# Kernel optimization log

Hardware: AMD Instinct MI355X
Metric: run time of the kernel (lower is better)

## Reference

```python
import jax, jax.numpy as jnp
import numpy as np

H = 128      # hidden_channels
G = 512      # number of graphs in the batch
NEG_SLOPE = 0.2


def _seg_sum(x, idx, n):
    return jax.ops.segment_sum(x, idx, num_segments=n)


def _sage(x_src, x_dst, ei, Wl, bl, Wr):
    # PyG SAGEConv: lin_l(mean_j x_j) + lin_r(x_i); lin_l has bias, lin_r does not.
    s, d = ei[0], ei[1]
    n = x_dst.shape[0]
    agg = _seg_sum(x_src[s], d, n)
    cnt = _seg_sum(jnp.ones((ei.shape[1],), x_src.dtype), d, n)
    mean = agg / jnp.maximum(cnt, 1.0)[:, None]
    return mean @ Wl + bl + x_dst @ Wr


def _gat(x_src, x_dst, ei, Ws, Wd, a_s, a_d, b):
    # PyG GATConv (heads=1, add_self_loops=False, bipartite): segment softmax over dst.
    s, d = ei[0], ei[1]
    n = x_dst.shape[0]
    hs = x_src @ Ws                                  # [N_src, H]
    hd = x_dst @ Wd                                  # [N_dst, H]
    logit = jax.nn.leaky_relu((hs @ a_s)[s] + (hd @ a_d)[d], NEG_SLOPE)
    m = jax.ops.segment_max(logit, d, num_segments=n)
    e = jnp.exp(logit - m[d])
    z = _seg_sum(e, d, n)
    alpha = e / jnp.maximum(z[d], 1e-16)
    return _seg_sum(alpha[:, None] * hs[s], d, n) + b


def _gcn(x, ei, W, b):
    # PyG GCNConv with add_self_loops=True, normalize=True (same src/dst node type).
    s, d = ei[0], ei[1]
    n = x.shape[0]
    deg = _seg_sum(jnp.ones((ei.shape[1],), x.dtype), d, n) + 1.0  # +1 self loop
    dis = jax.lax.rsqrt(deg)
    h = x @ W
    norm = dis[s] * dis[d]
    out = _seg_sum(norm[:, None] * h[s], d, n) + (dis * dis)[:, None] * h
    return out + b


def _pool(x, b):
    s = _seg_sum(x, b, G)
    c = _seg_sum(jnp.ones((x.shape[0],), x.dtype), b, G)
    return s / jnp.maximum(c, 1.0)[:, None]


def setup_inputs() -> dict:
    key = jax.random.key(0)
    ks = iter(jax.random.split(key, 80))
    scale = 1.0 / np.sqrt(H)

    def nrm(shape, sc=scale):
        return jax.random.normal(next(ks), shape, jnp.float32) * sc

    def edges(e, n_src, n_dst):
        src = jax.random.randint(next(ks), (e,), 0, n_src, jnp.int32)
        dst = jax.random.randint(next(ks), (e,), 0, n_dst, jnp.int32)
        return jnp.stack([src, dst])

    def batch(n):
        return jnp.sort(jax.random.randint(next(ks), (n,), 0, G, jnp.int32))

    N_CD, N_SEQ, N_ANNO, N_RANGE, N_MD = 100000, 80000, 80000, 80000, 50000
    inp = {
        'x_cd': nrm((N_CD, H), 1.0), 'x_seq': nrm((N_SEQ, H), 1.0),
        'x_anno': nrm((N_ANNO, H), 1.0), 'x_range': nrm((N_RANGE, H), 1.0),
        'x_md': nrm((N_MD, H), 1.0),
        'ei_seq': edges(160000, N_CD, N_SEQ),
        'ei_anno': edges(200000, N_CD, N_ANNO),
        'ei_range': edges(200000, N_CD, N_RANGE),
        'ei_comp': edges(300000, N_MD, N_CD),
        'ei_cc': edges(300000, N_CD, N_CD),
        'ei_mm': edges(150000, N_MD, N_MD),
        'b_cd': batch(N_CD), 'b_seq': batch(N_SEQ), 'b_anno': batch(N_ANNO),
        'b_range': batch(N_RANGE), 'b_md': batch(N_MD),
    }
    # per-layer stacked params (leading axis = 2 layers)
    for nm, shp in [('Wsl_seq', (2, H, H)), ('bs_seq', (2, H)), ('Wsr_seq', (2, H, H)),
                    ('Wsl_anno', (2, H, H)), ('bs_anno', (2, H)), ('Wsr_anno', (2, H, H)),
                    ('Wg_comp_s', (2, H, H)), ('Wg_comp_d', (2, H, H)),
                    ('ag_comp_s', (2, H)), ('ag_comp_d', (2, H)), ('bg_comp', (2, H)),
                    ('Wg_range_s', (2, H, H)), ('Wg_range_d', (2, H, H)),
                    ('ag_range_s', (2, H)), ('ag_range_d', (2, H)), ('bg_range', (2, H)),
                    ('Wc_cc', (2, H, H)), ('bc_cc', (2, H)),
                    ('Wc_mm', (2, H, H)), ('bc_mm', (2, H)),
                    ('lin1_W', (5 * H, H)), ('lin1_b', (H,)),
                    ('lin2_W', (H, 1)), ('lin2_b', (1,))]:
        inp[nm] = nrm(shp)
    return inp


def reference(x_cd, x_seq, x_anno, x_range, x_md,
              ei_seq, ei_anno, ei_range, ei_comp, ei_cc, ei_mm,
              b_cd, b_seq, b_anno, b_range, b_md,
              Wsl_seq, bs_seq, Wsr_seq, Wsl_anno, bs_anno, Wsr_anno,
              Wg_comp_s, Wg_comp_d, ag_comp_s, ag_comp_d, bg_comp,
              Wg_range_s, Wg_range_d, ag_range_s, ag_range_d, bg_range,
              Wc_cc, bc_cc, Wc_mm, bc_mm,
              lin1_W, lin1_b, lin2_W, lin2_b):
    for l in range(2):
        # HeteroConv aggr='sum': CD receives GAT(MD->CD) + GCN(CD->CD)
        n_cd = (_gat(x_md, x_cd, ei_comp, Wg_comp_s[l], Wg_comp_d[l],
                     ag_comp_s[l], ag_comp_d[l], bg_comp[l])
                + _gcn(x_cd, ei_cc, Wc_cc[l], bc_cc[l]))
        n_seq = _sage(x_cd, x_seq, ei_seq, Wsl_seq[l], bs_seq[l], Wsr_seq[l])
        n_anno = _sage(x_cd, x_anno, ei_anno, Wsl_anno[l], bs_anno[l], Wsr_anno[l])
        n_range = _gat(x_cd, x_range, ei_range, Wg_range_s[l], Wg_range_d[l],
                       ag_range_s[l], ag_range_d[l], bg_range[l])
        n_md = _gcn(x_md, ei_mm, Wc_mm[l], bc_mm[l])
        x_cd, x_seq, x_anno, x_range, x_md = (
            jax.nn.relu(n_cd), jax.nn.relu(n_seq), jax.nn.relu(n_anno),
            jax.nn.relu(n_range), jax.nn.relu(n_md))
    emb = jnp.concatenate([_pool(x_cd, b_cd), _pool(x_seq, b_seq),
                           _pool(x_anno, b_anno), _pool(x_range, b_range),
                           _pool(x_md, b_md)], axis=-1)        # [G, 5H]
    h = jax.nn.relu(emb @ lin1_W + lin1_b)  # Dropout(0.7) is identity in eval
    return (h @ lin2_W + lin2_b).reshape(-1)  # [G]
```

## Files before the change

kernel.cpp:

```cpp
#include <hip/hip_runtime.h>

#define HD 128
#define GNUM 512
#define RPB 520
#define IDXCAP 1024

typedef __attribute__((ext_vector_type(8))) short short8v;
typedef __attribute__((ext_vector_type(4))) float f32x4;

__device__ __forceinline__ void split1(float a, short& h, short& l) {
  unsigned u = __float_as_uint(a);
  unsigned hb = (u + 0x7FFFu + ((u >> 16) & 1u)) & 0xFFFF0000u;
  h = (short)(hb >> 16);
  float rest = a - __uint_as_float(hb);
  unsigned u2 = __float_as_uint(rest);
  l = (short)((u2 + 0x7FFFu + ((u2 >> 16) & 1u)) >> 16);
}

struct WTab { const float* p[8]; };
__global__ __launch_bounds__(256) void k_split_w(WTab tab, short* __restrict__ whi,
                                                 short* __restrict__ wlo)
{
  int m = blockIdx.x >> 6;
  int i = (blockIdx.x & 63) * 256 + threadIdx.x;
  const float* W = tab.p[m >> 1] + (m & 1) * 16384;
  int k = i >> 7, n = i & 127;
  short h, l;
  split1(W[k * 128 + n], h, l);
  whi[m * 16384 + n * 128 + k] = h;
  wlo[m * 16384 + n * 128 + k] = l;
}

#define CF_LD 132
__device__ __forceinline__ void gemm_body(
    int blockid, char* smem, int* idxbuf,
    const float* __restrict__ A1, const short* __restrict__ WH1, const short* __restrict__ WL1,
    const int* __restrict__ grp, const int* __restrict__ gcol,
    const float* __restrict__ A2, const short* __restrict__ WH2, const short* __restrict__ WL2,
    float* __restrict__ C, const float* __restrict__ bias, int N, int relu,
    const float* __restrict__ avec, float* __restrict__ adot)
{
  short* Ah = (short*)smem;
  short* Al = Ah + 64 * 136;
  float* Cf = (float*)smem;

  const int t = threadIdx.x;
  const int row0 = blockid * 64;
  const int lane = t & 63, wid = t >> 6;
  const int g = lane >> 4, cn = lane & 15;
  const int colbase = wid * 32;

  f32x4 zero = {0.f, 0.f, 0.f, 0.f};
  f32x4 acc[4][2];
#pragma unroll
  for (int rt = 0; rt < 4; ++rt) { acc[rt][0] = zero; acc[rt][1] = zero; }

  float4 a2reg[8];
  if (A2) {
    const float4* A4 = (const float4*)(A2 + (size_t)row0 * 128);
#pragma unroll
    for (int i = 0; i < 8; ++i) {
      int f4 = t + i * 256;
      int row = f4 >> 5;
      a2reg[i] = (row0 + row < N) ? A4[f4] : make_float4(0.f, 0.f, 0.f, 0.f);
    }
  }

  auto stageA = [&](const float* __restrict__ A) {
    const float4* A4 = (const float4*)(A + (size_t)row0 * 128);
#pragma unroll
    for (int i = 0; i < 8; ++i) {
      int f4 = t + i * 256;
      int row = f4 >> 5, c4 = f4 & 31;
      float4 v = make_float4(0.f, 0.f, 0.f, 0.f);
      if (row0 + row < N) v = A4[f4];
      short4 h, l;
      split1(v.x, h.x, l.x); split1(v.y, h.y, l.y);
      split1(v.z, h.z, l.z); split1(v.w, h.w, l.w);
      *(short4*)(Ah + row * 136 + c4 * 4) = h;
      *(short4*)(Al + row * 136 + c4 * 4) = l;
    }
  };

  auto stageA_gather = [&](const float* __restrict__ X, int e_lo) {
#pragma unroll
    for (int i = 0; i < 8; ++i) {
      int f4 = t + i * 256;
      int row = f4 >> 5, ln = f4 & 31;
      int r = row0 + row;
      float4 s = make_float4(0.f, 0.f, 0.f, 0.f);
      int e0 = 0, e1 = 0;
      if (r < N) { e0 = grp[r]; e1 = grp[r + 1]; }
      for (int e = e0; e < e1; ++e) {
        int off = e - e_lo;
        int c = (off < IDXCAP) ? idxbuf[off] : gcol[e];
        float4 v = *(const float4*)(X + (size_t)c * 128 + ln * 4);
        s.x += v.x; s.y += v.y; s.z += v.z; s.w += v.w;
      }
      float inv = 1.f / fmaxf((float)(e1 - e0), 1.f);
      short4 h, l;
      split1(s.x * inv, h.x, l.x); split1(s.y * inv, h.y, l.y);
      split1(s.z * inv, h.z, l.z); split1(s.w * inv, h.w, l.w);
      *(short4*)(Ah + row * 136 + ln * 4) = h;
      *(short4*)(Al + row * 136 + ln * 4) = l;
    }
  };

  auto accum = [&](const short* __restrict__ WH, const short* __restrict__ WL) {
    short8v bhi[2][4], blo[2][4];
#pragma unroll
    for (int ct = 0; ct < 2; ++ct)
#pragma unroll
      for (int kg = 0; kg < 4; ++kg) {
        size_t o = (size_t)(colbase + ct * 16 + cn) * 128 + kg * 32 + g * 8;
        bhi[ct][kg] = *(const short8v*)(WH + o);
        blo[ct][kg] = *(const short8v*)(WL + o);
      }
#pragma unroll
    for (int kg = 0; kg < 4; ++kg) {
#pragma unroll
      for (int rt = 0; rt < 4; ++rt) {
        const int ao = (rt * 16 + cn) * 136 + kg * 32 + g * 8;
        const short8v ah = *(const short8v*)(Ah + ao);
        const short8v al = *(const short8v*)(Al + ao);
#pragma unroll
        for (int ct = 0; ct < 2; ++ct) {
          acc[rt][ct] = __builtin_amdgcn_mfma_f32_16x16x32_bf16(ah, bhi[ct][kg], acc[rt][ct], 0, 0, 0);
          acc[rt][ct] = __builtin_amdgcn_mfma_f32_16x16x32_bf16(al, bhi[ct][kg], acc[rt][ct], 0, 0, 0);
          acc[rt][ct] = __builtin_amdgcn_mfma_f32_16x16x32_bf16(ah, blo[ct][kg], acc[rt][ct], 0, 0, 0);
        }
      }
    }
  };

  if (grp) {
    const int row_end = min(row0 + 64, N);
    const int e_lo = grp[row0];
    const int cnt = min(grp[row_end] - e_lo, IDXCAP);
    for (int k = t; k < cnt; k += 256) idxbuf[k] = gcol[e_lo + k];
    __syncthreads();
    stageA_gather(A1, e_lo);
  } else {
    stageA(A1);
  }
  __syncthreads();
  accum(WH1, WL1);
  if (A2) {
    __syncthreads();
#pragma unroll
    for (int i = 0; i < 8; ++i) {
      int f4 = t + i * 256;
      int row = f4 >> 5, c4 = f4 & 31;
      short4 h, l;
      split1(a2reg[i].x, h.x, l.x); split1(a2reg[i].y, h.y, l.y);
      split1(a2reg[i].z, h.z, l.z); split1(a2reg[i].w, h.w, l.w);
      *(short4*)(Ah + row * 136 + c4 * 4) = h;
      *(short4*)(Al + row * 136 + c4 * 4) = l;
    }
    __syncthreads();
    accum(WH2, WL2);
  }
  __syncthreads();

  if (avec) {
    float* part = (float*)smem;
    const float av0 = avec[colbase + cn];
    const float av1 = avec[colbase + 16 + cn];
#pragma unroll
    for (int rt = 0; rt < 4; ++rt)
#pragma unroll
      for (int r = 0; r < 4; ++r) {
        float p = fmaf(acc[rt][1][r], av1, acc[rt][0][r] * av0);
#pragma unroll
        for (int o = 1; o < 16; o <<= 1) p += __shfl_xor(p, o);
        if (cn == 0) part[wid * 64 + rt * 16 + g * 4 + r] = p;
      }
    __syncthreads();
    if (t < 64) {
      int row = row0 + t;
      if (row < N) adot[row] = part[t] + part[64 + t] + part[128 + t] + part[192 + t];
    }
    __syncthreads();
  }

#pragma unroll
  for (int rt = 0; rt < 4; ++rt)
#pragma unroll
    for (int ct = 0; ct < 2; ++ct)
#pragma unroll
      for (int r = 0; r < 4; ++r)
        Cf[(rt * 16 + g * 4 + r) * CF_LD + colbase + ct * 16 + cn] = acc[rt][ct][r];
  __syncthreads();

  float4* C4 = (float4*)(C + (size_t)row0 * 128);
#pragma unroll
  for (int i = 0; i < 8; ++i) {
    int f4 = t + i * 256;
    int row = f4 >> 5, c4 = f4 & 31;
    if (row0 + row < N) {
      float4 v = *(const float4*)(Cf + row * CF_LD + c4 * 4);
      if (bias) {
        float4 bv = *(const float4*)(bias + c4 * 4);
        v.x += bv.x; v.y += bv.y; v.z += bv.z; v.w += bv.w;
      }
      if (relu) {
        v.x = fmaxf(v.x, 0.f); v.y = fmaxf(v.y, 0.f);
        v.z = fmaxf(v.z, 0.f); v.w = fmaxf(v.w, 0.f);
      }
      C4[f4] = v;
    }
  }
}

__global__ __launch_bounds__(256) void k_gemm_mfma(
    const float* A1, const short* WH1, const short* WL1,
    const int* grp, const int* gcol,
    const float* A2, const short* WH2, const short* WL2,
    float* C, const float* bias, int N, int relu,
    const float* avec, float* adot)
{
  __shared__ char smem[64 * 136 * 2 * 2];
  __shared__ int idxbuf[IDXCAP];
  gemm_body(blockIdx.x, smem, idxbuf, A1, WH1, WL1, grp, gcol,
            A2, WH2, WL2, C, bias, N, relu, avec, adot);
}

struct SPair {
  const float* A1[2]; const short* WH1[2]; const short* WL1[2];
  const int* grp[2]; const int* gcol[2];
  const float* A2[2]; const short* WH2[2]; const short* WL2[2];
  float* C[2]; const float* bias[2]; int N[2]; int bo;
};
__global__ __launch_bounds__(256) void k_gemm_sage2(SPair p)
{
  __shared__ char smem[64 * 136 * 2 * 2];
  __shared__ int idxbuf[IDXCAP];
  int ty = (blockIdx.x >= p.bo) ? 1 : 0;
  int bid = blockIdx.x - (ty ? p.bo : 0);
  gemm_body(bid, smem, idxbuf, p.A1[ty], p.WH1[ty], p.WL1[ty], p.grp[ty], p.gcol[ty],
            p.A2[ty], p.WH2[ty], p.WL2[ty], p.C[ty], p.bias[ty], p.N[ty], 1,
            nullptr, nullptr);
}

__global__ void k_rowdot(const float* __restrict__ x, const float* __restrict__ a,
                         float* __restrict__ out, int N)
{
  int wid = blockIdx.x * 4 + (threadIdx.x >> 6);
  int lane = threadIdx.x & 63;
  if (wid >= N) return;
  float2 xv = ((const float2*)x)[(size_t)wid * 64 + lane];
  float2 av = ((const float2*)a)[lane];
  float v = fmaf(xv.y, av.y, xv.x * av.x);
#pragma unroll
  for (int o = 32; o > 0; o >>= 1) v += __shfl_down(v, o);
  if (lane == 0) out[wid] = v;
}

struct MTab { const float* W[4]; const float* a[4]; };
__global__ __launch_bounds__(128) void k_matvec4(MTab tb, float* __restrict__ wv)
{
  __shared__ float as[128];
  int m = blockIdx.x, i = threadIdx.x;
  as[i] = tb.a[m][i];
  __syncthreads();
  const float* W = tb.W[m];
  float v = 0.f;
  for (int j = 0; j < 128; ++j) v = fmaf(W[i * 128 + j], as[j], v);
  wv[m * 128 + i] = v;
}

struct HTab { const int* key[6]; int* cnt[6]; unsigned short* rank[6]; int bo[7]; int n[6]; };
__global__ void k_hist_rank_all(HTab tb) {
  int bi = blockIdx.x, ty = 0;
  while (ty < 5 && bi >= tb.bo[ty + 1]) ++ty;
  int i = (bi - tb.bo[ty]) * 256 + threadIdx.x;
  if (i < tb.n[ty])
    tb.rank[ty][i] = (unsigned short)atomicAdd(&tb.cnt[ty][tb.key[ty][i]], 1);
}

struct FTab { const int* es[6]; const int* ed[6]; const int* rp[6];
              const unsigned short* rank[6]; int* col[6]; int bo[7]; int n[6]; };
__global__ void k_fill_all(FTab tb) {
  int bi = blockIdx.x, ty = 0;
  while (ty < 5 && bi >= tb.bo[ty + 1]) ++ty;
  int e = (bi - tb.bo[ty]) * 256 + threadIdx.x;
  if (e >= tb.n[ty]) return;
  int p = tb.rp[ty][tb.ed[ty][e]] + (int)tb.rank[ty][e];
  tb.col[ty][p] = tb.es[ty][e];
}

struct STab { int* rp[6]; int* bs[6]; int n[6]; int bo[7]; };

__global__ __launch_bounds__(256) void k_scan_partial_all(STab tb) {
  __shared__ int red[256];
  int bi = blockIdx.x, ty = 0;
  while (ty < 5 && bi >= tb.bo[ty + 1]) ++ty;
  int lb = bi - tb.bo[ty];
  const int* rp = tb.rp[ty];
  const int N = tb.n[ty];
  const int t = threadIdx.x, base = lb * 4096;
  int s = 0;
  for (int i = t; i < 4096; i += 256) {
    int idx = base + i;
    if (idx < N) s += rp[idx];
  }
  red[t] = s;
  __syncthreads();
  for (int ofs = 128; ofs > 0; ofs >>= 1) {
    if (t < ofs) red[t] += red[t + ofs];
    __syncthreads();
  }
  if (t == 0) tb.bs[ty][lb] = red[0];
}

__global__ __launch_bounds__(256) void k_scan_bsums_all(STab tb) {
  __shared__ int sh[256];
  const int ty = blockIdx.x;
  const int nb = (tb.n[ty] + 4095) / 4096;
  const int t = threadIdx.x;
  int v = (t < nb) ? tb.bs[ty][t] : 0;
  sh[t] = v;
  __syncthreads();
  for (int ofs = 1; ofs < 256; ofs <<= 1) {
    int u = (t >= ofs) ? sh[t - ofs] : 0;
    __syncthreads();
    sh[t] += u;
    __syncthreads();
  }
  if (t < nb) tb.bs[ty][t] = sh[t] - v;
  if (t == 255) tb.rp[ty][tb.n[ty]] = sh[255];
}

__global__ __launch_bounds__(256) void k_scan_final_all(STab tb) {
  __shared__ int sh[4096 + 256];
  __shared__ int tsum[256];
  int bi = blockIdx.x, ty = 0;
  while (ty < 5 && bi >= tb.bo[ty + 1]) ++ty;
  int lb = bi - tb.bo[ty];
  int* rp = tb.rp[ty];
  const int N = tb.n[ty];
  const int t = threadIdx.x, base = lb * 4096;
  auto mp = [](int i) { return i + (i >> 4); };
#pragma unroll
  for (int i = 0; i < 16; ++i) {
    int idx = base + i * 256 + t;
    sh[mp(i * 256 + t)] = (idx < N) ? rp[idx] : 0;
  }
  __syncthreads();
  int s = 0;
#pragma unroll
  for (int j = 0; j < 16; ++j) s += sh[mp(t * 16 + j)];
  tsum[t] = s;
  __syncthreads();
  for (int ofs = 1; ofs < 256; ofs <<= 1) {
    int u = (t >= ofs) ? tsum[t - ofs] : 0;
    __syncthreads();
    tsum[t] += u;
    __syncthreads();
  }
  int pre = tsum[t] - s + tb.bs[ty][lb];
#pragma unroll
  for (int j = 0; j < 16; ++j) {
    int v = sh[mp(t * 16 + j)];
    sh[mp(t * 16 + j)] = pre;
    pre += v;
  }
  __syncthreads();
#pragma unroll
  for (int i = 0; i < 16; ++i) {
    int idx = base + i * 256 + t;
    if (idx < N) rp[idx] = sh[mp(i * 256 + t)];
  }
}

struct BTab { const int* b[5]; int n[5]; };
__global__ __launch_bounds__(512) void k_runptr(BTab tb, int* __restrict__ rpb_all) {
  const int ty = blockIdx.x;
  const int* b = tb.b[ty];
  const int N = tb.n[ty];
  const int t = threadIdx.x;
  int lo = 0, hi = N;
  while (lo < hi) {
    int mid = (lo + hi) >> 1;
    if (b[mid] < t) lo = mid + 1; else hi = mid;
  }
  rpb_all[ty * RPB + t] = lo;
  if (t == 0) rpb_all[ty * RPB + GNUM] = N;
}

struct DTab { const int* rp[2]; float* dis[2]; int n[2]; int bo[3]; };
__global__ void k_dis2(DTab tb) {
  int bi = blockIdx.x, ty = (bi >= tb.bo[1]) ? 1 : 0;
  int n = (bi - tb.bo[ty]) * 256 + threadIdx.x;
  if (n < tb.n[ty]) tb.dis[ty][n] = rsqrtf((float)(tb.rp[ty][n + 1] - tb.rp[ty][n]) + 1.f);
}

__global__ void k_gcn_gather(const int* __restrict__ rp, const int* __restrict__ col,
                             const float* __restrict__ dis, const float* __restrict__ h,
                             const float* addin, const float* __restrict__ b,
                             float* out, int N,
                             const float* __restrict__ dvec, float* __restrict__ dout)
{
  int node = blockIdx.x * 4 + (threadIdx.x >> 6);
  if (node >= N) return;
  int lane = threadIdx.x & 63;
  int s0 = rp[node], deg = rp[node + 1] - s0;
  float rd = dis[node];
  const float2* h2 = (const float2*)h;
  float2 hself = h2[(size_t)node * 64 + lane];
  float2 bv = ((const float2*)b)[lane];
  float ad0 = 0.f, ad1 = 0.f;
  if (addin) {
    float2 a2 = ((const float2*)addin)[(size_t)node * 64 + lane];
    ad0 = a2.x; ad1 = a2.y;
  }
  float a0 = 0.f, a1 = 0.f, b0 = 0.f, b1 = 0.f;
  for (int base = 0; base < deg; base += 64) {
    int m = min(64, deg - base);
    int c = 0; float dv = 0.f;
    if (lane < m) { c = col[s0 + base + lane]; dv = dis[c]; }
    int j = 0;
    for (; j + 1 < m; j += 2) {
      int sA = __shfl(c, j), sB = __shfl(c, j + 1);
      float nA = __shfl(dv, j) * rd, nB = __shfl(dv, j + 1) * rd;
      float2 vA = h2[(size_t)sA * 64 + lane];
      float2 vB = h2[(size_t)sB * 64 + lane];
      a0 = fmaf(nA, vA.x, a0); a1 = fmaf(nA, vA.y, a1);
      b0 = fmaf(nB, vB.x, b0); b1 = fmaf(nB, vB.y, b1);
    }
    if (j < m) {
      int sA = __shfl(c, j);
      float nA = __shfl(dv, j) * rd;
      float2 vA = h2[(size_t)sA * 64 + lane];
      a0 = fmaf(nA, vA.x, a0); a1 = fmaf(nA, vA.y, a1);
    }
  }
  float rr = rd * rd;
  float v0 = fmaf(rr, hself.x, a0 + b0) + bv.x + ad0;
  float v1 = fmaf(rr, hself.y, a1 + b1) + bv.y + ad1;
  v0 = fmaxf(v0, 0.f); v1 = fmaxf(v1, 0.f);
  ((float2*)out)[(size_t)node * 64 + lane] = make_float2(v0, v1);
  if (dvec) {
    float2 wv = ((const float2*)dvec)[lane];
    float p = fmaf(v1, wv.y, v0 * wv.x);
#pragma unroll
    for (int o = 32; o > 0; o >>= 1) p += __shfl_xor(p, o);
    if (lane == 0) dout[node] = p;
  }
}

__global__ void k_gat_gather(const int* __restrict__ rp, const int* __restrict__ col,
                             const float* __restrict__ hs, const float* __restrict__ as_,
                             const float* __restrict__ ad_, const float* __restrict__ b,
                             float* __restrict__ out, int N, int relu,
                             const float* __restrict__ dvec, float* __restrict__ dout)
{
  int node = blockIdx.x * 4 + (threadIdx.x >> 6);
  if (node >= N) return;
  int lane = threadIdx.x & 63;
  int s0 = rp[node], deg = rp[node + 1] - s0;
  float adn = ad_[node];
  float2 bv = ((const float2*)b)[lane];
  const float2* hs2 = (const float2*)hs;
  float z = 0.f, a0 = 0.f, a1 = 0.f, b0 = 0.f, b1 = 0.f;
  for (int base = 0; base < deg; base += 64) {
    int m = min(64, deg - base);
    int c = 0; float av = 0.f;
    if (lane < m) { c = col[s0 + base + lane]; av = as_[c]; }
    int j = 0;
    for (; j + 1 < m; j += 2) {
      int sA = __shfl(c, j), sB = __shfl(c, j + 1);
      float vA = __shfl(av, j) + adn, vB = __shfl(av, j + 1) + adn;
      vA = vA > 0.f ? vA : 0.2f * vA;
      vB = vB > 0.f ? vB : 0.2f * vB;
      float pA = __expf(vA), pB = __expf(vB);
      z += pA + pB;
      float2 hA = hs2[(size_t)sA * 64 + lane];
      float2 hB = hs2[(size_t)sB * 64 + lane];
      a0 = fmaf(pA, hA.x, a0); a1 = fmaf(pA, hA.y, a1);
      b0 = fmaf(pB, hB.x, b0); b1 = fmaf(pB, hB.y, b1);
    }
    if (j < m) {
      int sA = __shfl(c, j);
      float vA = __shfl(av, j) + adn;
      vA = vA > 0.f ? vA : 0.2f * vA;
      float pA = __expf(vA);
      z += pA;
      float2 hA = hs2[(size_t)sA * 64 + lane];
      a0 = fmaf(pA, hA.x, a0); a1 = fmaf(pA, hA.y, a1);
    }
  }
  float inv = (deg > 0) ? 1.f / z : 0.f;
  float v0 = fmaf(a0 + b0, inv, bv.x);
  float v1 = fmaf(a1 + b1, inv, bv.y);
  if (relu) { v0 = fmaxf(v0, 0.f); v1 = fmaxf(v1, 0.f); }
  ((float2*)out)[(size_t)node * 64 + lane] = make_float2(v0, v1);
  if (dvec) {
    float2 wv = ((const float2*)dvec)[lane];
    float p = fmaf(v1, wv.y, v0 * wv.x);
#pragma unroll
    for (int o = 32; o > 0; o >>= 1) p += __shfl_xor(p, o);
    if (lane == 0) dout[node] = p;
  }
}

__global__ __launch_bounds__(256) void k_pool_seg(
    const float* __restrict__ x, const int* __restrict__ rpb,
    float* __restrict__ pool, int col_off)
{
  __shared__ float2 red2[4][64];
  const int g = blockIdx.x;
  const int t = threadIdx.x, w = t >> 6, lane = t & 63;
  const int n0 = rpb[g], n1 = rpb[g + 1];
  const float2* x2 = (const float2*)x;
  float a0 = 0.f, a1 = 0.f, b0 = 0.f, b1 = 0.f;
  int n = n0 + w;
  for (; n + 4 < n1; n += 8) {
    float2 vA = x2[(size_t)n * 64 + lane];
    float2 vB = x2[(size_t)(n + 4) * 64 + lane];
    a0 += vA.x; a1 += vA.y; b0 += vB.x; b1 += vB.y;
  }
  if (n < n1) { float2 vA = x2[(size_t)n * 64 + lane]; a0 += vA.x; a1 += vA.y; }
  red2[w][lane] = make_float2(a0 + b0, a1 + b1);
  __syncthreads();
  if (t < 64) {
    float2 r0 = red2[0][t], r1 = red2[1][t], r2 = red2[2][t], r3 = red2[3][t];
    float inv = 1.f / fmaxf((float)(n1 - n0), 1.f);
    ((float2*)(pool + (size_t)g * 640 + col_off))[t] =
        make_float2((r0.x + r1.x + r2.x + r3.x) * inv,
                    (r0.y + r1.y + r2.y + r3.y) * inv);
  }
}

__global__ void k_mlp(const float* __restrict__ pool,
                      const float* __restrict__ W1, const float* __restrict__ b1,
                      const float* __restrict__ W2, const float* __restrict__ b2,
                      float* __restrict__ out)
{
  __shared__ float emb[640];
  __shared__ float red[128];
  const int g = blockIdx.x, t = threadIdx.x;
  for (int i = t; i < 640; i += 128) emb[i] = pool[(size_t)g * 640 + i];
  __syncthreads();
  float acc = b1[t];
  for (int i = 0; i < 640; ++i) acc = fmaf(emb[i], W1[i * 128 + t], acc);
  float h = fmaxf(acc, 0.f);
  red[t] = h * W2[t];
  __syncthreads();
  for (int s = 64; s > 0; s >>= 1) {
    if (t < s) red[t] += red[t + s];
    __syncthreads();
  }
  if (t == 0) out[g] = red[0] + b2[0];
}

extern "C" void kernel_launch(void* const* d_in, const int* in_sizes, int n_in,
                              void* d_out, int out_size, void* d_ws, size_t ws_size,
                              hipStream_t stream)
{
  auto fin = [&](int i) { return (const float*)d_in[i]; };
  auto iin = [&](int i) { return (const int*)d_in[i]; };

  const float *x_cd = fin(0), *x_seq = fin(1), *x_anno = fin(2), *x_range = fin(3), *x_md = fin(4);
  const int *ei_seq = iin(5), *ei_anno = iin(6), *ei_range = iin(7),
            *ei_comp = iin(8), *ei_cc = iin(9), *ei_mm = iin(10);
  const int *b_cd = iin(11), *b_seq = iin(12), *b_anno = iin(13), *b_range = iin(14), *b_md = iin(15);

  const int N_CD = in_sizes[0] / HD, N_SEQ = in_sizes[1] / HD, N_ANNO = in_sizes[2] / HD,
            N_RANGE = in_sizes[3] / HD, N_MD = in_sizes[4] / HD;
  const int E_seq = in_sizes[5] / 2, E_anno = in_sizes[6] / 2, E_range = in_sizes[7] / 2,
            E_comp = in_sizes[8] / 2, E_cc = in_sizes[9] / 2, E_mm = in_sizes[10] / 2;
  const int N_OTH = max(max(N_SEQ, N_ANNO), N_RANGE);

  auto WLm = [&](int i, int l) { return fin(i) + (size_t)l * HD * HD; };
  auto WLv = [&](int i, int l) { return fin(i) + (size_t)l * HD; };

  float* ws = (float*)d_ws;
  size_t off = 0;
  auto alloc = [&](size_t n) { float* p = ws + off; off += (n + 3) & ~(size_t)3; return p; };
  float* xcd1 = alloc((size_t)N_CD * HD);
  float* xmd1 = alloc((size_t)N_MD * HD);
  float* xoth = alloc((size_t)N_OTH * HD);
  float* acc  = alloc((size_t)N_CD * HD);
  float* t1   = alloc((size_t)N_CD * HD);
  float* sAs  = alloc((size_t)N_CD);
  float* sAd  = alloc((size_t)N_CD);
  float* sAd2 = alloc((size_t)N_CD);
  float* dis_cc = alloc((size_t)N_CD);
  float* dis_mm = alloc((size_t)N_MD);
  float* wvall = alloc(4 * HD);
  float* pool = alloc((size_t)GNUM * 5 * HD);
  short* whi = (short*)(ws + off); off += (size_t)16 * 16384 / 2;
  short* wlo = (short*)(ws + off); off += (size_t)16 * 16384 / 2;
  auto alloci = [&](size_t n) { int* p = (int*)(ws + off); off += (n + 3) & ~(size_t)3; return p; };
  int* bsall = alloci(6 * 256);
  int* rpb_all = alloci(5 * RPB);
  int Nds[6] = {N_SEQ, N_ANNO, N_RANGE, N_CD, N_CD, N_MD};
  int Es[6]  = {E_seq, E_anno, E_range, E_comp, E_cc, E_mm};
  int* rps[6];
  int* rp0 = alloci(0);
  { size_t tot = 0; for (int i = 0; i < 6; ++i) tot += (size_t)Nds[i] + 1;
    int* p = alloci(tot); rp0 = p;
    for (int i = 0; i < 6; ++i) { rps[i] = p; p += Nds[i] + 1; } }
  size_t rp_tot_bytes = 0; for (int i = 0; i < 6; ++i) rp_tot_bytes += ((size_t)Nds[i] + 1) * 4;
  unsigned short* ranks[6];
  for (int i = 0; i < 6; ++i) ranks[i] = (unsigned short*)alloci(((size_t)Es[i] + 1) / 2);
  int* cols[6];  for (int i = 0; i < 6; ++i) cols[i] = alloci((size_t)Es[i]);
  (void)n_in;

  if (off * sizeof(float) > ws_size) {
    hipMemsetAsync(d_out, 0, (size_t)out_size * sizeof(float), stream);
    return;
  }

  auto ew = [&](size_t elems) { return dim3((unsigned)((elems + 255) / 256)); };
  auto nw = [&](int N) { return dim3((unsigned)((N + 3) / 4)); };

  WTab tab;
  tab.p[0] = fin(16); tab.p[1] = fin(18); tab.p[2] = fin(19); tab.p[3] = fin(21);
  tab.p[4] = fin(22); tab.p[5] = fin(27); tab.p[6] = fin(32); tab.p[7] = fin(34);
  k_split_w<<<dim3(1024), dim3(256), 0, stream>>>(tab, whi, wlo);

  MTab mt;
  mt.W[0] = WLm(23, 0); mt.a[0] = WLv(25, 0);
  mt.W[1] = WLm(23, 1); mt.a[1] = WLv(25, 1);
  mt.W[2] = WLm(28, 0); mt.a[2] = WLv(30, 0);
  mt.W[3] = WLm(28, 1); mt.a[3] = WLv(30, 1);
  k_matvec4<<<dim3(4), dim3(128), 0, stream>>>(mt, wvall);

  {
    BTab bt;
    bt.b[0] = b_cd; bt.n[0] = N_CD;  bt.b[1] = b_seq; bt.n[1] = N_SEQ;
    bt.b[2] = b_anno; bt.n[2] = N_ANNO;  bt.b[3] = b_range; bt.n[3] = N_RANGE;
    bt.b[4] = b_md; bt.n[4] = N_MD;
    k_runptr<<<dim3(5), dim3(512), 0, stream>>>(bt, rpb_all);
  }

  const int* ess[6] = {ei_seq, ei_anno, ei_range, ei_comp, ei_cc, ei_mm};
  const int* eds[6] = {ei_seq + E_seq, ei_anno + E_anno, ei_range + E_range,
                       ei_comp + E_comp, ei_cc + E_cc, ei_mm + E_mm};
  hipMemsetAsync(rp0, 0, rp_tot_bytes, stream);
  {
    HTab ht; int b = 0;
    for (int i = 0; i < 6; ++i) {
      ht.key[i] = eds[i]; ht.cnt[i] = rps[i]; ht.rank[i] = ranks[i];
      ht.bo[i] = b; b += (Es[i] + 255) / 256; ht.n[i] = Es[i];
    }
    ht.bo[6] = b;
    k_hist_rank_all<<<dim3(b), dim3(256), 0, stream>>>(ht);
  }
  {
    STab st; int b = 0;
    for (int i = 0; i < 6; ++i) {
      st.rp[i] = rps[i]; st.bs[i] = bsall + i * 256;
      st.n[i] = Nds[i]; st.bo[i] = b; b += (Nds[i] + 4095) / 4096;
    }
    st.bo[6] = b;
    k_scan_partial_all<<<dim3(b), dim3(256), 0, stream>>>(st);
    k_scan_bsums_all<<<dim3(6), dim3(256), 0, stream>>>(st);
    k_scan_final_all<<<dim3(b), dim3(256), 0, stream>>>(st);
  }
  {
    FTab ft; int b = 0;
    for (int i = 0; i < 6; ++i) {
      ft.es[i] = ess[i]; ft.ed[i] = eds[i]; ft.rp[i] = rps[i]; ft.rank[i] = ranks[i];
      ft.col[i] = cols[i]; ft.bo[i] = b; b += (Es[i] + 255) / 256; ft.n[i] = Es[i];
    }
    ft.bo[6] = b;
    k_fill_all<<<dim3(b), dim3(256), 0, stream>>>(ft);
  }
  int *rp_seq = rps[0], *rp_anno = rps[1], *rp_range = rps[2],
      *rp_comp = rps[3], *rp_cc = rps[4], *rp_mm = rps[5];
  int *col_seq = cols[0], *col_anno = cols[1], *col_range = cols[2],
      *col_comp = cols[3], *col_cc = cols[4], *col_mm = cols[5];
  {
    DTab dt;
    dt.rp[0] = rp_cc; dt.dis[0] = dis_cc; dt.n[0] = N_CD;
    dt.rp[1] = rp_mm; dt.dis[1] = dis_mm; dt.n[1] = N_MD;
    dt.bo[0] = 0; dt.bo[1] = (N_CD + 255) / 256;
    dt.bo[2] = dt.bo[1] + (N_MD + 255) / 256;
    k_dis2<<<dim3(dt.bo[2]), dim3(256), 0, stream>>>(dt);
  }

  auto WHp = [&](int sidx, int layer) { return whi + (size_t)(sidx * 2 + layer) * 16384; };
  auto WLp = [&](int sidx, int layer) { return wlo + (size_t)(sidx * 2 + layer) * 16384; };
  auto gemm = [&](const float* A, int sidx, int layer, float* C, const float* b,
                  int N, int relu, const float* avec = nullptr, float* adot = nullptr) {
    k_gemm_mfma<<<dim3((N + 63) / 64), dim3(256), 0, stream>>>(
        A, WHp(sidx, layer), WLp(sidx, layer), nullptr, nullptr,
        nullptr, nullptr, nullptr, C, b, N, relu, avec, adot);
  };
  auto sage2 = [&](const float* g0, const int* rp0_, const int* gc0, const float* s0,
                   float* C0, const float* b0, int N0, int sl0, int sr0,
                   const float* g1, const int* rp1_, const int* gc1, const float* s1,
                   float* C1, const float* b1, int N1, int sl1, int sr1, int layer) {
    SPair p;
    p.A1[0] = g0; p.grp[0] = rp0_; p.gcol[0] = gc0; p.A2[0] = s0;
    p.WH1[0] = WHp(sl0, layer); p.WL1[0] = WLp(sl0, layer);
    p.WH2[0] = WHp(sr0, layer); p.WL2[0] = WLp(sr0, layer);
    p.C[0] = C0; p.bias[0] = b0; p.N[0] = N0;
    p.A1[1] = g1; p.grp[1] = rp1_; p.gcol[1] = gc1; p.A2[1] = s1;
    p.WH1[1] = WHp(sl1, layer); p.WL1[1] = WLp(sl1, layer);
    p.WH2[1] = WHp(sr1, layer); p.WL2[1] = WLp(sr1, layer);
    p.C[1] = C1; p.bias[1] = b1; p.N[1] = N1;
    p.bo = (N0 + 63) / 64;
    int total = p.bo + (N1 + 63) / 64;
    k_gemm_sage2<<<dim3(total), dim3(256), 0, stream>>>(p);
  };
  auto do_pool = [&](const float* x, int type) {
    k_pool_seg<<<dim3(GNUM), dim3(256), 0, stream>>>(x, rpb_all + type * RPB, pool, type * HD);
  };

  auto gat = [&](const float* xs, const float* xd, const int* rp, const int* col,
                 int Ns, int Nd, int sidx, int layer, const float* avs_raw,
                 const float* sAd_src, int wvD,
                 const float* dvec, float* dout,
                 const float* bias, float* out, int relu) {
    if (wvD >= 0) {
      k_rowdot<<<nw(Nd), dim3(256), 0, stream>>>(xd, wvall + wvD * 128, sAd, Nd);
      sAd_src = sAd;
    }
    gemm(xs, sidx, layer, t1, nullptr, Ns, 0, avs_raw, sAs);
    k_gat_gather<<<nw(Nd), dim3(256), 0, stream>>>(rp, col, t1, sAs, sAd_src, bias,
                                                   out, Nd, relu, dvec, dout);
  };
  auto gcn = [&](const float* x, const int* rp, const int* col, const float* dis, int N,
                 int sidx, int layer, const float* b, const float* addin, float* out,
                 const float* dvec, float* dout) {
    gemm(x, sidx, layer, t1, nullptr, N, 0);
    k_gcn_gather<<<nw(N), dim3(256), 0, stream>>>(rp, col, dis, t1, addin, b, out, N,
                                                  dvec, dout);
  };

  gat(x_md, x_cd, rp_comp, col_comp, N_MD, N_CD, 4, 0, WLv(24, 0),
      nullptr, 0, nullptr, nullptr, WLv(26, 0), acc, 0);
  gcn(x_cd, rp_cc, col_cc, dis_cc, N_CD, 6, 0, WLv(33, 0), acc, xcd1,
      wvall + 1 * 128, sAd2);
  gcn(x_md, rp_mm, col_mm, dis_mm, N_MD, 7, 0, WLv(35, 0), nullptr, xmd1,
      nullptr, nullptr);
  gat(xmd1, xcd1, rp_comp, col_comp, N_MD, N_CD, 4, 1, WLv(24, 1),
      sAd2, -1, nullptr, nullptr, WLv(26, 1), acc, 0);
  gcn(xcd1, rp_cc, col_cc, dis_cc, N_CD, 6, 1, WLv(33, 1), acc, acc,
      nullptr, nullptr);
  do_pool(acc, 0);
  gcn(xmd1, rp_mm, col_mm, dis_mm, N_MD, 7, 1, WLv(35, 1), nullptr, acc,
      nullptr, nullptr);
  do_pool(acc, 4);

  sage2(x_cd, rp_seq, col_seq, x_seq, xoth, WLv(17, 0), N_SEQ, 0, 1,
        x_cd, rp_anno, col_anno, x_anno, t1, WLv(20, 0), N_ANNO, 2, 3, 0);
  sage2(xcd1, rp_seq, col_seq, xoth, xoth, WLv(17, 1), N_SEQ, 0, 1,
        xcd1, rp_anno, col_anno, t1, t1, WLv(20, 1), N_ANNO, 2, 3, 1);
  do_pool(xoth, 1);
  do_pool(t1, 2);

  gat(x_cd, x_range, rp_range, col_range, N_CD, N_RANGE, 5, 0, WLv(29, 0),
      nullptr, 2, wvall + 3 * 128, sAd2, WLv(31, 0), xoth, 1);
  gat(xcd1, xoth, rp_range, col_range, N_CD, N_RANGE, 5, 1, WLv(29, 1),
      sAd2, -1, nullptr, nullptr, WLv(31, 1), acc, 1);
  do_pool(acc, 3);

  k_mlp<<<dim3(GNUM), dim3(128), 0, stream>>>(
      pool, fin(36), fin(37), fin(38), fin(39), (float*)d_out);
}
```

Measured before the change: 1.033 ms.

## Parallelize SAGE mean-gather over edges with LDS atomics instead of per-row loops

The fused gather+GEMM stage for SAGE no longer has each thread walk one row's edge list serially. Each wave now takes edges round-robin, loads a full 128-float source row, finds the destination row by binary search over CSR offsets cached in shared memory, and accumulates into an fp32 LDS tile with atomicAdd. Afterwards the tile is scaled by inverse degree and split to bf16 hi/lo for the MFMA path. This is meant to balance work across skewed degrees and make the gathers more coalesced, at the cost of LDS atomic contention, a binary search per edge and extra barriers.

```diff
diff --git a/kernel.cpp b/kernel.cpp
--- a/kernel.cpp
+++ b/kernel.cpp
@@ -33,7 +33,7 @@
 
 #define CF_LD 132
 __device__ __forceinline__ void gemm_body(
-    int blockid, char* smem, int* idxbuf,
+    int blockid, char* smem, int* idxbuf, int* rpsh,
     const float* __restrict__ A1, const short* __restrict__ WH1, const short* __restrict__ WL1,
     const int* __restrict__ grp, const int* __restrict__ gcol,
     const float* __restrict__ A2, const short* __restrict__ WH2, const short* __restrict__ WL2,
@@ -82,30 +82,6 @@
     }
   };
 
-  auto stageA_gather = [&](const float* __restrict__ X, int e_lo) {
-#pragma unroll
-    for (int i = 0; i < 8; ++i) {
-      int f4 = t + i * 256;
-      int row = f4 >> 5, ln = f4 & 31;
-      int r = row0 + row;
-      float4 s = make_float4(0.f, 0.f, 0.f, 0.f);
-      int e0 = 0, e1 = 0;
-      if (r < N) { e0 = grp[r]; e1 = grp[r + 1]; }
-      for (int e = e0; e < e1; ++e) {
-        int off = e - e_lo;
-        int c = (off < IDXCAP) ? idxbuf[off] : gcol[e];
-        float4 v = *(const float4*)(X + (size_t)c * 128 + ln * 4);
-        s.x += v.x; s.y += v.y; s.z += v.z; s.w += v.w;
-      }
-      float inv = 1.f / fmaxf((float)(e1 - e0), 1.f);
-      short4 h, l;
-      split1(s.x * inv, h.x, l.x); split1(s.y * inv, h.y, l.y);
-      split1(s.z * inv, h.z, l.z); split1(s.w * inv, h.w, l.w);
-      *(short4*)(Ah + row * 136 + ln * 4) = h;
-      *(short4*)(Al + row * 136 + ln * 4) = l;
-    }
-  };
-
   auto accum = [&](const short* __restrict__ WH, const short* __restrict__ WL) {
     short8v bhi[2][4], blo[2][4];
 #pragma unroll
@@ -134,12 +110,47 @@
   };
 
   if (grp) {
-    const int row_end = min(row0 + 64, N);
+    const int row_end = min(64, N - row0);
     const int e_lo = grp[row0];
-    const int cnt = min(grp[row_end] - e_lo, IDXCAP);
+    const int e_hi = grp[row0 + row_end];
+    const int nE = e_hi - e_lo;
+    const int cnt = min(nE, IDXCAP);
+    if (t <= row_end) rpsh[t] = grp[row0 + t];
     for (int k = t; k < cnt; k += 256) idxbuf[k] = gcol[e_lo + k];
-    __syncthreads();
-    stageA_gather(A1, e_lo);
+    float* Acc = Cf;
+    for (int k = t; k < 64 * CF_LD; k += 256) Acc[k] = 0.f;
+    __syncthreads();
+    for (int e = wid; e < nE; e += 4) {
+      int c = (e < IDXCAP) ? idxbuf[e] : gcol[e_lo + e];
+      float2 v = ((const float2*)(A1 + (size_t)c * 128))[lane];
+      int ge = e_lo + e;
+      int lo = 0, hi = row_end;
+      while (hi - lo > 1) { int mid = (lo + hi) >> 1; if (rpsh[mid] <= ge) lo = mid; else hi = mid; }
+      atomicAdd(&Acc[lo * CF_LD + lane * 2], v.x);
+      atomicAdd(&Acc[lo * CF_LD + lane * 2 + 1], v.y);
+    }
+    __syncthreads();
+    float4 rowreg[8];
+#pragma unroll
+    for (int i = 0; i < 8; ++i) {
+      int f4 = t + i * 256;
+      int row = f4 >> 5, c4 = f4 & 31;
+      float4 v = *(const float4*)(Acc + row * CF_LD + c4 * 4);
+      int deg = (row < row_end) ? (rpsh[row + 1] - rpsh[row]) : 0;
+      float inv = 1.f / fmaxf((float)deg, 1.f);
+      rowreg[i] = make_float4(v.x * inv, v.y * inv, v.z * inv, v.w * inv);
+    }
+    __syncthreads();
+#pragma unroll
+    for (int i = 0; i < 8; ++i) {
+      int f4 = t + i * 256;
+      int row = f4 >> 5, c4 = f4 & 31;
+      short4 h, l;
+      split1(rowreg[i].x, h.x, l.x); split1(rowreg[i].y, h.y, l.y);
+      split1(rowreg[i].z, h.z, l.z); split1(rowreg[i].w, h.w, l.w);
+      *(short4*)(Ah + row * 136 + c4 * 4) = h;
+      *(short4*)(Al + row * 136 + c4 * 4) = l;
+    }
   } else {
     stageA(A1);
   }
@@ -221,7 +232,8 @@
 {
   __shared__ char smem[64 * 136 * 2 * 2];
   __shared__ int idxbuf[IDXCAP];
-  gemm_body(blockIdx.x, smem, idxbuf, A1, WH1, WL1, grp, gcol,
+  __shared__ int rpsh[65];
+  gemm_body(blockIdx.x, smem, idxbuf, rpsh, A1, WH1, WL1, grp, gcol,
             A2, WH2, WL2, C, bias, N, relu, avec, adot);
 }
 
@@ -235,9 +247,10 @@
 {
   __shared__ char smem[64 * 136 * 2 * 2];
   __shared__ int idxbuf[IDXCAP];
+  __shared__ int rpsh[65];
   int ty = (blockIdx.x >= p.bo) ? 1 : 0;
   int bid = blockIdx.x - (ty ? p.bo : 0);
-  gemm_body(bid, smem, idxbuf, p.A1[ty], p.WH1[ty], p.WL1[ty], p.grp[ty], p.gcol[ty],
+  gemm_body(bid, smem, idxbuf, rpsh, p.A1[ty], p.WH1[ty], p.WL1[ty], p.grp[ty], p.gcol[ty],
             p.A2[ty], p.WH2[ty], p.WL2[ty], p.C[ty], p.bias[ty], p.N[ty], 1,
             nullptr, nullptr);
 }
```

New measurement: 1.514 ms. 46.6% more time.
